# Kernel tuning notes

Hardware: AMD Instinct MI355X
Metric: run time of the kernel (lower is better)

## Reference

```python
import jax, jax.numpy as jnp
import numpy as np

N_NODES = 50000
N_EDGES = 800000
C_IN = 64
N_HEADS = 4
HEAD_DIM = 16
FC = 64


def setup_inputs() -> dict:
    key = jax.random.key(0)
    ks = jax.random.split(key, 20)
    d = {}
    d["node_input"] = jax.random.normal(ks[0], (N_NODES, C_IN), jnp.float32)
    d["node_attr"] = jnp.ones((N_NODES, 1), jnp.float32)
    d["edge_src"] = jax.random.randint(ks[1], (N_EDGES,), 0, N_NODES)
    d["edge_dst"] = jax.random.randint(ks[2], (N_EDGES,), 0, N_NODES)
    d["edge_attr"] = jax.random.normal(ks[3], (N_EDGES, 1), jnp.float32)
    d["edge_scalars"] = jax.random.normal(ks[4], (N_EDGES, FC), jnp.float32)
    d["batch"] = jnp.zeros((N_NODES,), jnp.int32)
    s = 1.0 / np.sqrt(C_IN)
    AD = N_HEADS * HEAD_DIM  # 64
    d["Wq"] = jax.random.normal(ks[5], (C_IN, AD), jnp.float32) * s
    d["bq"] = jnp.zeros((AD,), jnp.float32)
    d["W_src"] = jax.random.normal(ks[6], (C_IN, C_IN), jnp.float32) * s
    d["b_src"] = jnp.zeros((C_IN,), jnp.float32)
    d["W_dst"] = jax.random.normal(ks[7], (C_IN, C_IN), jnp.float32) * s
    d["W_fc1"] = jax.random.normal(ks[8], (FC, FC), jnp.float32) * (1.0 / np.sqrt(FC))
    d["b_fc1"] = jnp.zeros((FC,), jnp.float32)
    d["W_fc2"] = jax.random.normal(ks[9], (FC, FC), jnp.float32) * (1.0 / np.sqrt(FC))
    d["b_fc2"] = jnp.zeros((FC,), jnp.float32)
    d["W_fc3"] = jax.random.normal(ks[10], (FC, C_IN), jnp.float32) * (1.0 / np.sqrt(FC))
    d["b_fc3"] = jnp.zeros((C_IN,), jnp.float32)
    d["W_kv"] = jax.random.normal(ks[11], (C_IN, 2 * AD), jnp.float32) * s
    d["b_kv"] = jnp.zeros((2 * AD,), jnp.float32)
    d["W_proj"] = jax.random.normal(ks[12], (AD, C_IN), jnp.float32) * (1.0 / np.sqrt(AD))
    d["b_proj"] = jnp.zeros((C_IN,), jnp.float32)
    return d


def reference(node_input, node_attr, edge_src, edge_dst, edge_attr, edge_scalars, batch,
              Wq, bq, W_src, b_src, W_dst, W_fc1, b_fc1, W_fc2, b_fc2, W_fc3, b_fc3,
              W_kv, b_kv, W_proj, b_proj):
    N = node_input.shape[0]
    # query: linear -> heads -> scale (ScaleFactor for HxH 0e irreps = 1/sqrt(num_irreps))
    q = (node_input @ Wq + bq).reshape(N, N_HEADS, HEAD_DIM)
    q = q * (1.0 / jnp.sqrt(jnp.float32(HEAD_DIM)))
    # edge messages
    msg_src = node_input @ W_src + b_src
    msg_dst = node_input @ W_dst
    kv = msg_src[edge_src] + msg_dst[edge_dst]  # [E, C]
    # SeparableFCTP (scalar irreps): radial MLP -> depthwise weights, x * edge_attr, linear
    h = jax.nn.silu(edge_scalars @ W_fc1 + b_fc1)
    h = jax.nn.silu(h @ W_fc2 + b_fc2)
    w = h @ W_fc3 + b_fc3  # [E, C] depthwise TP weights
    tp = kv * edge_attr * w
    kv2 = (tp @ W_kv + b_kv).reshape(-1, 2 * N_HEADS, HEAD_DIM)
    k = kv2[:, :N_HEADS]
    v = kv2[:, N_HEADS:]
    # per-edge scores and segment softmax over incoming edges of each dst node
    alpha = jnp.einsum('ehd,ehd->eh', q[edge_dst], k)  # [E, H]
    seg_max = jax.ops.segment_max(alpha, edge_dst, num_segments=N)
    seg_max = jnp.where(jnp.isfinite(seg_max), seg_max, 0.0)
    ex = jnp.exp(alpha - seg_max[edge_dst])
    denom = jax.ops.segment_sum(ex, edge_dst, num_segments=N)
    alpha = ex / (denom[edge_dst] + 1e-16)
    # weighted scatter-sum of values
    attn = jax.ops.segment_sum(v * alpha[..., None], edge_dst, num_segments=N)
    attn = attn.reshape(N, N_HEADS * HEAD_DIM)
    return attn @ W_proj + b_proj
```

## Files before the change

### kernel.cpp

```cpp
#include <hip/hip_runtime.h>
#include <hip/hip_bf16.h>


typedef __attribute__((ext_vector_type(8))) short    bf16x8;
typedef __attribute__((ext_vector_type(4))) float    f32x4;
typedef __attribute__((ext_vector_type(4))) unsigned short ushort4v;

__device__ __forceinline__ unsigned short f2bf(float x) {
    union { float f; unsigned u; } v; v.f = x;
    unsigned r = v.u + 0x7fffu + ((v.u >> 16) & 1u);
    return (unsigned short)(r >> 16);
}

__device__ __forceinline__ int swz(int row, int k) {
    return row * 64 + (k ^ ((row & 7) << 3));
}

__device__ __forceinline__ bf16x8 ldfrag(const unsigned short* buf, int rn, int kk, int lhi) {
    return *(const bf16x8*)(buf + swz(rn, kk * 32 + lhi * 8));
}

__global__ __launch_bounds__(384)
void node_linear_kernel(const float* __restrict__ x,
                        const float* __restrict__ Wq,   const float* __restrict__ bq,
                        const float* __restrict__ Wsrc, const float* __restrict__ bsrc,
                        const float* __restrict__ Wdst,
                        float* __restrict__ qout, float* __restrict__ msout,
                        float* __restrict__ mdout, int N)
{
    __shared__ __align__(16) float sW[64 * 192];
    __shared__ float sb[192];
    __shared__ __align__(16) float xs[32][68];

    const int t = threadIdx.x;
    for (int idx4 = t; idx4 < 3072; idx4 += 384) {
        const int k  = idx4 / 48;
        const int j4 = idx4 % 48;
        const float4* src = (j4 < 16) ? (const float4*)&Wq  [k * 64 + j4 * 4]
                         : (j4 < 32) ? (const float4*)&Wsrc[k * 64 + (j4 - 16) * 4]
                                     : (const float4*)&Wdst[k * 64 + (j4 - 32) * 4];
        ((float4*)sW)[idx4] = *src;
    }
    if (t < 192) sb[t] = (t < 64) ? bq[t] : (t < 128) ? bsrc[t - 64] : 0.0f;

    const int nbase = blockIdx.x * 32;
    for (int idx = t; idx < 512; idx += 384) {
        const int n  = idx >> 4;
        const int c4 = (idx & 15) * 4;
        const int gn = nbase + n;
        float4 g = make_float4(0.f, 0.f, 0.f, 0.f);
        if (gn < N) g = *(const float4*)&x[(size_t)gn * 64 + c4];
        *(float4*)&xs[n][c4] = g;
    }
    __syncthreads();

    const int te = t / 48, tj = t % 48;
    const int j0 = tj * 4, e0 = te * 4;

    float acc[4][4];
#pragma unroll
    for (int i = 0; i < 4; ++i)
#pragma unroll
        for (int c = 0; c < 4; ++c) acc[i][c] = 0.f;

#pragma unroll 16
    for (int k = 0; k < 64; ++k) {
        const float4 wv = *(const float4*)&sW[k * 192 + j0];
        const float a0 = xs[e0 + 0][k], a1 = xs[e0 + 1][k];
        const float a2 = xs[e0 + 2][k], a3 = xs[e0 + 3][k];
        acc[0][0] += a0 * wv.x; acc[0][1] += a0 * wv.y; acc[0][2] += a0 * wv.z; acc[0][3] += a0 * wv.w;
        acc[1][0] += a1 * wv.x; acc[1][1] += a1 * wv.y; acc[1][2] += a1 * wv.z; acc[1][3] += a1 * wv.w;
        acc[2][0] += a2 * wv.x; acc[2][1] += a2 * wv.y; acc[2][2] += a2 * wv.z; acc[2][3] += a2 * wv.w;
        acc[3][0] += a3 * wv.x; acc[3][1] += a3 * wv.y; acc[3][2] += a3 * wv.z; acc[3][3] += a3 * wv.w;
    }

#pragma unroll
    for (int i = 0; i < 4; ++i) {
        const int gn = nbase + e0 + i;
        if (gn >= N) continue;
        float4 o;
        o.x = acc[i][0] + sb[j0 + 0];
        o.y = acc[i][1] + sb[j0 + 1];
        o.z = acc[i][2] + sb[j0 + 2];
        o.w = acc[i][3] + sb[j0 + 3];
        if (j0 < 64) {
            o.x *= 0.25f; o.y *= 0.25f; o.z *= 0.25f; o.w *= 0.25f;
            *(float4*)&qout[(size_t)gn * 64 + j0] = o;
        } else if (j0 < 128) {
            *(float4*)&msout[(size_t)gn * 64 + (j0 - 64)] = o;
        } else {
            *(float4*)&mdout[(size_t)gn * 64 + (j0 - 128)] = o;
        }
    }
}

__global__ __launch_bounds__(512, 4)
void edge_fused_mfma(const int* __restrict__ esrc, const int* __restrict__ edst,
                     const float* __restrict__ eattr, const float* __restrict__ escal,
                     const float* __restrict__ W1, const float* __restrict__ b1,
                     const float* __restrict__ W2, const float* __restrict__ b2,
                     const float* __restrict__ W3, const float* __restrict__ b3,
                     const float* __restrict__ Wkv, const float* __restrict__ bkv,
                     const float* __restrict__ qbuf, const float* __restrict__ msrc,
                     const float* __restrict__ mdst,
                     float* __restrict__ num, float* __restrict__ den)
{
    __shared__ __align__(16) unsigned short sh[36864];
    unsigned short* sW1t  = sh;
    unsigned short* sW2t  = sh + 4096;
    unsigned short* sW3t  = sh + 8192;
    unsigned short* sWkvt = sh + 12288;
    unsigned short* sA0   = sh + 20480;
    unsigned short* sA1   = sh + 28672;
    __shared__ float sB1[64], sB2[64], sB3[64], sBkv[128], sEa[128];
    __shared__ int   sSrc[128], sDst[128];

    const int t    = threadIdx.x;
    const int base = blockIdx.x * 128;
    const int lane = t & 63;
    const int wave = t >> 6;
    const int l15  = lane & 15;
    const int lhi  = lane >> 4;
    const int rowBase = wave * 16;

    for (int idx = t; idx < 4096; idx += 512) {
        const int k = idx >> 6, n = idx & 63;
        const int d = swz(n, k);
        sW1t[d] = f2bf(W1[idx]);
        sW2t[d] = f2bf(W2[idx]);
        sW3t[d] = f2bf(W3[idx]);
    }
    for (int idx = t; idx < 8192; idx += 512) {
        const int k = idx >> 7, n = idx & 127;
        sWkvt[swz(n, k)] = f2bf(Wkv[idx]);
    }
    for (int i4 = t; i4 < 2048; i4 += 512) {
        const int e = i4 >> 4, k4 = (i4 & 15) << 2;
        const float4 g = *(const float4*)&escal[(size_t)(base + e) * 64 + k4];
        ushort4v p = { f2bf(g.x), f2bf(g.y), f2bf(g.z), f2bf(g.w) };
        *(ushort4v*)&sA0[swz(e, k4)] = p;
    }
    if (t < 64)              { sB1[t] = b1[t]; sB2[t] = b2[t]; sB3[t] = b3[t]; }
    if (t >= 64  && t < 192) sBkv[t - 64] = bkv[t - 64];
    if (t >= 192 && t < 320) {
        const int e = t - 192;
        sSrc[e] = esrc[base + e];
        sDst[e] = edst[base + e];
        sEa[e]  = eattr[base + e];
    }
    __syncthreads();

    {
        f32x4 acc[4] = {{0,0,0,0},{0,0,0,0},{0,0,0,0},{0,0,0,0}};
#pragma unroll
        for (int kk = 0; kk < 2; ++kk) {
            const bf16x8 a = ldfrag(sA0, rowBase + l15, kk, lhi);
#pragma unroll
            for (int c = 0; c < 4; ++c) {
                const bf16x8 b = ldfrag(sW1t, c * 16 + l15, kk, lhi);
                acc[c] = __builtin_amdgcn_mfma_f32_16x16x32_bf16(a, b, acc[c], 0, 0, 0);
            }
        }
#pragma unroll
        for (int c = 0; c < 4; ++c)
#pragma unroll
            for (int r = 0; r < 4; ++r) {
                const int row = rowBase + lhi * 4 + r;
                const int col = c * 16 + l15;
                const float v = acc[c][r] + sB1[col];
                sA1[swz(row, col)] = f2bf(v / (1.f + __expf(-v)));
            }
    }
    __syncthreads();

    {
        f32x4 acc[4] = {{0,0,0,0},{0,0,0,0},{0,0,0,0},{0,0,0,0}};
#pragma unroll
        for (int kk = 0; kk < 2; ++kk) {
            const bf16x8 a = ldfrag(sA1, rowBase + l15, kk, lhi);
#pragma unroll
            for (int c = 0; c < 4; ++c) {
                const bf16x8 b = ldfrag(sW2t, c * 16 + l15, kk, lhi);
                acc[c] = __builtin_amdgcn_mfma_f32_16x16x32_bf16(a, b, acc[c], 0, 0, 0);
            }
        }
#pragma unroll
        for (int c = 0; c < 4; ++c)
#pragma unroll
            for (int r = 0; r < 4; ++r) {
                const int row = rowBase + lhi * 4 + r;
                const int col = c * 16 + l15;
                const float v = acc[c][r] + sB2[col];
                sA0[swz(row, col)] = f2bf(v / (1.f + __expf(-v)));
            }
    }
    __syncthreads();

    {
        f32x4 acc[4] = {{0,0,0,0},{0,0,0,0},{0,0,0,0},{0,0,0,0}};
#pragma unroll
        for (int kk = 0; kk < 2; ++kk) {
            const bf16x8 a = ldfrag(sA0, rowBase + l15, kk, lhi);
#pragma unroll
            for (int c = 0; c < 4; ++c) {
                const bf16x8 b = ldfrag(sW3t, c * 16 + l15, kk, lhi);
                acc[c] = __builtin_amdgcn_mfma_f32_16x16x32_bf16(a, b, acc[c], 0, 0, 0);
            }
        }
        float ms[4][4], md[4][4];
#pragma unroll
        for (int c = 0; c < 4; ++c)
#pragma unroll
            for (int r = 0; r < 4; ++r) {
                const int row = rowBase + lhi * 4 + r;
                const int col = c * 16 + l15;
                ms[c][r] = msrc[(size_t)sSrc[row] * 64 + col];
                md[c][r] = mdst[(size_t)sDst[row] * 64 + col];
            }
#pragma unroll
        for (int c = 0; c < 4; ++c)
#pragma unroll
            for (int r = 0; r < 4; ++r) {
                const int row = rowBase + lhi * 4 + r;
                const int col = c * 16 + l15;
                const float w  = acc[c][r] + sB3[col];
                const float tp = (ms[c][r] + md[c][r]) * sEa[row] * w;
                sA1[swz(row, col)] = f2bf(tp);
            }
    }
    __syncthreads();

    f32x4 acc2[8] = {{0,0,0,0},{0,0,0,0},{0,0,0,0},{0,0,0,0},
                     {0,0,0,0},{0,0,0,0},{0,0,0,0},{0,0,0,0}};
#pragma unroll
    for (int kk = 0; kk < 2; ++kk) {
        const bf16x8 a = ldfrag(sA1, rowBase + l15, kk, lhi);
#pragma unroll
        for (int c = 0; c < 8; ++c) {
            const bf16x8 b = ldfrag(sWkvt, c * 16 + l15, kk, lhi);
            acc2[c] = __builtin_amdgcn_mfma_f32_16x16x32_bf16(a, b, acc2[c], 0, 0, 0);
        }
    }

    int   gds[4];
    float qreg[4][4];
#pragma unroll
    for (int r = 0; r < 4; ++r) gds[r] = sDst[rowBase + lhi * 4 + r];
#pragma unroll
    for (int h = 0; h < 4; ++h)
#pragma unroll
        for (int r = 0; r < 4; ++r)
            qreg[h][r] = qbuf[(size_t)gds[r] * 64 + h * 16 + l15];

    float ex[4][4];
#pragma unroll
    for (int h = 0; h < 4; ++h)
#pragma unroll
        for (int r = 0; r < 4; ++r) {
            float s = (acc2[h][r] + sBkv[h * 16 + l15]) * qreg[h][r];
            s += __shfl_xor(s, 1);
            s += __shfl_xor(s, 2);
            s += __shfl_xor(s, 4);
            s += __shfl_xor(s, 8);
            const float e = __expf(s);
            ex[h][r] = e;
            if (l15 == h * 4 + r) atomicAdd(&den[(size_t)gds[r] * 4 + h], e);
        }

#pragma unroll
    for (int vt = 0; vt < 4; ++vt)
#pragma unroll
        for (int r = 0; r < 4; ++r) {
            const float vv = acc2[4 + vt][r] + sBkv[64 + vt * 16 + l15];
            atomicAdd(&num[(size_t)gds[r] * 64 + vt * 16 + l15], ex[vt][r] * vv);
        }
}

__global__ __launch_bounds__(256)
void final_proj_kernel(const float* __restrict__ num, const float* __restrict__ den,
                       const float* __restrict__ Wp, const float* __restrict__ bp,
                       float* __restrict__ out, int N)
{
    __shared__ __align__(16) float sW[64 * 64];
    __shared__ float sb[64];
    __shared__ __align__(16) float at[64][68];

    const int t = threadIdx.x;
    for (int i4 = t; i4 < 1024; i4 += 256)
        ((float4*)sW)[i4] = ((const float4*)Wp)[i4];
    if (t < 64) sb[t] = bp[t];

    const int nbase = blockIdx.x * 64;
    for (int idx = t; idx < 1024; idx += 256) {
        const int n  = idx >> 4;
        const int c4 = (idx & 15) * 4;
        const int gn = nbase + n;
        float4 g = make_float4(0.f, 0.f, 0.f, 0.f);
        if (gn < N) {
            const float4 nm = *(const float4*)&num[(size_t)gn * 64 + c4];
            const float inv = 1.0f / (den[(size_t)gn * 4 + (c4 >> 4)] + 1e-16f);
            g = make_float4(nm.x * inv, nm.y * inv, nm.z * inv, nm.w * inv);
        }
        *(float4*)&at[n][c4] = g;
    }
    __syncthreads();

    const int te = t >> 4, tj = t & 15;
    const int j0 = tj * 4, e0 = te * 4;

    float acc[4][4];
#pragma unroll
    for (int i = 0; i < 4; ++i)
#pragma unroll
        for (int c = 0; c < 4; ++c) acc[i][c] = 0.f;

#pragma unroll 16
    for (int k = 0; k < 64; ++k) {
        const float4 wv = *(const float4*)&sW[k * 64 + j0];
        const float a0 = at[e0 + 0][k], a1 = at[e0 + 1][k];
        const float a2 = at[e0 + 2][k], a3 = at[e0 + 3][k];
        acc[0][0] += a0 * wv.x; acc[0][1] += a0 * wv.y; acc[0][2] += a0 * wv.z; acc[0][3] += a0 * wv.w;
        acc[1][0] += a1 * wv.x; acc[1][1] += a1 * wv.y; acc[1][2] += a1 * wv.z; acc[1][3] += a1 * wv.w;
        acc[2][0] += a2 * wv.x; acc[2][1] += a2 * wv.y; acc[2][2] += a2 * wv.z; acc[2][3] += a2 * wv.w;
        acc[3][0] += a3 * wv.x; acc[3][1] += a3 * wv.y; acc[3][2] += a3 * wv.z; acc[3][3] += a3 * wv.w;
    }

#pragma unroll
    for (int i = 0; i < 4; ++i) {
        const int gn = nbase + e0 + i;
        if (gn >= N) continue;
        float4 o;
        o.x = acc[i][0] + sb[j0 + 0];
        o.y = acc[i][1] + sb[j0 + 1];
        o.z = acc[i][2] + sb[j0 + 2];
        o.w = acc[i][3] + sb[j0 + 3];
        *(float4*)&out[(size_t)gn * 64 + j0] = o;
    }
}

extern "C" void kernel_launch(void* const* d_in, const int* in_sizes, int n_in,
                              void* d_out, int out_size, void* d_ws, size_t ws_size,
                              hipStream_t stream)
{
    const float* node_input = (const float*)d_in[0];
    const int*   edge_src   = (const int*)  d_in[2];
    const int*   edge_dst   = (const int*)  d_in[3];
    const float* edge_attr  = (const float*)d_in[4];
    const float* edge_scal  = (const float*)d_in[5];
    const float* Wq    = (const float*)d_in[7];
    const float* bq    = (const float*)d_in[8];
    const float* W_src = (const float*)d_in[9];
    const float* b_src = (const float*)d_in[10];
    const float* W_dst = (const float*)d_in[11];
    const float* W_fc1 = (const float*)d_in[12];
    const float* b_fc1 = (const float*)d_in[13];
    const float* W_fc2 = (const float*)d_in[14];
    const float* b_fc2 = (const float*)d_in[15];
    const float* W_fc3 = (const float*)d_in[16];
    const float* b_fc3 = (const float*)d_in[17];
    const float* W_kv  = (const float*)d_in[18];
    const float* b_kv  = (const float*)d_in[19];
    const float* W_proj = (const float*)d_in[20];
    const float* b_proj = (const float*)d_in[21];

    const int N = in_sizes[0] / 64;
    const int E = in_sizes[2];

    float* ws    = (float*)d_ws;
    float* q_buf = ws;
    float* msrc  = ws + (size_t)N * 64;
    float* mdst  = ws + (size_t)N * 128;
    float* num   = ws + (size_t)N * 192;
    float* den   = ws + (size_t)N * 256;

    hipMemsetAsync(num, 0, (size_t)N * 68 * sizeof(float), stream);

    {
        dim3 grid((N + 31) / 32);
        node_linear_kernel<<<grid, 384, 0, stream>>>(node_input, Wq, bq, W_src, b_src, W_dst,
                                                     q_buf, msrc, mdst, N);
    }
    {
        dim3 grid(E / 128);
        edge_fused_mfma<<<grid, 512, 0, stream>>>(edge_src, edge_dst, edge_attr, edge_scal,
                                                  W_fc1, b_fc1, W_fc2, b_fc2, W_fc3, b_fc3,
                                                  W_kv, b_kv, q_buf, msrc, mdst, num, den);
    }
    {
        dim3 grid((N + 63) / 64);
        final_proj_kernel<<<grid, 256, 0, stream>>>(num, den, W_proj, b_proj, (float*)d_out, N);
    }
}
```

Before: 730.2 us.

## Persistent grid-stride kernels with precomputed swizzled bf16 weights

```diff
diff --git a/kernel.cpp b/kernel.cpp
--- a/kernel.cpp
+++ b/kernel.cpp
@@ -18,6 +18,27 @@
 
 __device__ __forceinline__ bf16x8 ldfrag(const unsigned short* buf, int rn, int kk, int lhi) {
     return *(const bf16x8*)(buf + swz(rn, kk * 32 + lhi * 8));
+}
+
+__global__ __launch_bounds__(256)
+void prep_weights(const float* __restrict__ W1, const float* __restrict__ W2,
+                  const float* __restrict__ W3, const float* __restrict__ Wkv,
+                  unsigned short* __restrict__ wbf)
+{
+    const int d = blockIdx.x * 256 + threadIdx.x;
+    if (d < 12288) {
+        const int w  = d >> 12;
+        const int r  = d & 4095;
+        const int n  = r >> 6, kx = r & 63;
+        const int k  = kx ^ ((n & 7) << 3);
+        const float* W = (w == 0) ? W1 : (w == 1) ? W2 : W3;
+        wbf[d] = f2bf(W[k * 64 + n]);
+    } else if (d < 20480) {
+        const int r  = d - 12288;
+        const int n  = r >> 6, kx = r & 63;
+        const int k  = kx ^ ((n & 7) << 3);
+        wbf[d] = f2bf(Wkv[k * 128 + n]);
+    }
 }
 
 __global__ __launch_bounds__(384)
@@ -26,7 +47,7 @@
                         const float* __restrict__ Wsrc, const float* __restrict__ bsrc,
                         const float* __restrict__ Wdst,
                         float* __restrict__ qout, float* __restrict__ msout,
-                        float* __restrict__ mdout, int N)
+                        float* __restrict__ mdout, int N, int ntiles)
 {
     __shared__ __align__(16) float sW[64 * 192];
     __shared__ float sb[192];
@@ -43,53 +64,56 @@
     }
     if (t < 192) sb[t] = (t < 64) ? bq[t] : (t < 128) ? bsrc[t - 64] : 0.0f;
 
-    const int nbase = blockIdx.x * 32;
-    for (int idx = t; idx < 512; idx += 384) {
-        const int n  = idx >> 4;
-        const int c4 = (idx & 15) * 4;
-        const int gn = nbase + n;
-        float4 g = make_float4(0.f, 0.f, 0.f, 0.f);
-        if (gn < N) g = *(const float4*)&x[(size_t)gn * 64 + c4];
-        *(float4*)&xs[n][c4] = g;
-    }
-    __syncthreads();
-
     const int te = t / 48, tj = t % 48;
     const int j0 = tj * 4, e0 = te * 4;
 
-    float acc[4][4];
-#pragma unroll
-    for (int i = 0; i < 4; ++i)
-#pragma unroll
-        for (int c = 0; c < 4; ++c) acc[i][c] = 0.f;
+    for (int tile = blockIdx.x; tile < ntiles; tile += gridDim.x) {
+        const int nbase = tile * 32;
+        __syncthreads();
+        for (int idx = t; idx < 512; idx += 384) {
+            const int n  = idx >> 4;
+            const int c4 = (idx & 15) * 4;
+            const int gn = nbase + n;
+            float4 g = make_float4(0.f, 0.f, 0.f, 0.f);
+            if (gn < N) g = *(const float4*)&x[(size_t)gn * 64 + c4];
+            *(float4*)&xs[n][c4] = g;
+        }
+        __syncthreads();
+
+        float acc[4][4];
+#pragma unroll
+        for (int i = 0; i < 4; ++i)
+#pragma unroll
+            for (int c = 0; c < 4; ++c) acc[i][c] = 0.f;
 
 #pragma unroll 16
-    for (int k = 0; k < 64; ++k) {
-        const float4 wv = *(const float4*)&sW[k * 192 + j0];
-        const float a0 = xs[e0 + 0][k], a1 = xs[e0 + 1][k];
-        const float a2 = xs[e0 + 2][k], a3 = xs[e0 + 3][k];
-        acc[0][0] += a0 * wv.x; acc[0][1] += a0 * wv.y; acc[0][2] += a0 * wv.z; acc[0][3] += a0 * wv.w;
-        acc[1][0] += a1 * wv.x; acc[1][1] += a1 * wv.y; acc[1][2] += a1 * wv.z; acc[1][3] += a1 * wv.w;
-        acc[2][0] += a2 * wv.x; acc[2][1] += a2 * wv.y; acc[2][2] += a2 * wv.z; acc[2][3] += a2 * wv.w;
-        acc[3][0] += a3 * wv.x; acc[3][1] += a3 * wv.y; acc[3][2] += a3 * wv.z; acc[3][3] += a3 * wv.w;
-    }
-
-#pragma unroll
-    for (int i = 0; i < 4; ++i) {
-        const int gn = nbase + e0 + i;
-        if (gn >= N) continue;
-        float4 o;
-        o.x = acc[i][0] + sb[j0 + 0];
-        o.y = acc[i][1] + sb[j0 + 1];
-        o.z = acc[i][2] + sb[j0 + 2];
-        o.w = acc[i][3] + sb[j0 + 3];
-        if (j0 < 64) {
-            o.x *= 0.25f; o.y *= 0.25f; o.z *= 0.25f; o.w *= 0.25f;
-            *(float4*)&qout[(size_t)gn * 64 + j0] = o;
-        } else if (j0 < 128) {
-            *(float4*)&msout[(size_t)gn * 64 + (j0 - 64)] = o;
-        } else {
-            *(float4*)&mdout[(size_t)gn * 64 + (j0 - 128)] = o;
+        for (int k = 0; k < 64; ++k) {
+            const float4 wv = *(const float4*)&sW[k * 192 + j0];
+            const float a0 = xs[e0 + 0][k], a1 = xs[e0 + 1][k];
+            const float a2 = xs[e0 + 2][k], a3 = xs[e0 + 3][k];
+            acc[0][0] += a0 * wv.x; acc[0][1] += a0 * wv.y; acc[0][2] += a0 * wv.z; acc[0][3] += a0 * wv.w;
+            acc[1][0] += a1 * wv.x; acc[1][1] += a1 * wv.y; acc[1][2] += a1 * wv.z; acc[1][3] += a1 * wv.w;
+            acc[2][0] += a2 * wv.x; acc[2][1] += a2 * wv.y; acc[2][2] += a2 * wv.z; acc[2][3] += a2 * wv.w;
+            acc[3][0] += a3 * wv.x; acc[3][1] += a3 * wv.y; acc[3][2] += a3 * wv.z; acc[3][3] += a3 * wv.w;
+        }
+
+#pragma unroll
+        for (int i = 0; i < 4; ++i) {
+            const int gn = nbase + e0 + i;
+            if (gn >= N) continue;
+            float4 o;
+            o.x = acc[i][0] + sb[j0 + 0];
+            o.y = acc[i][1] + sb[j0 + 1];
+            o.z = acc[i][2] + sb[j0 + 2];
+            o.w = acc[i][3] + sb[j0 + 3];
+            if (j0 < 64) {
+                o.x *= 0.25f; o.y *= 0.25f; o.z *= 0.25f; o.w *= 0.25f;
+                *(float4*)&qout[(size_t)gn * 64 + j0] = o;
+            } else if (j0 < 128) {
+                *(float4*)&msout[(size_t)gn * 64 + (j0 - 64)] = o;
+            } else {
+                *(float4*)&mdout[(size_t)gn * 64 + (j0 - 128)] = o;
+            }
         }
     }
 }
@@ -97,13 +121,12 @@
 __global__ __launch_bounds__(512, 4)
 void edge_fused_mfma(const int* __restrict__ esrc, const int* __restrict__ edst,
                      const float* __restrict__ eattr, const float* __restrict__ escal,
-                     const float* __restrict__ W1, const float* __restrict__ b1,
-                     const float* __restrict__ W2, const float* __restrict__ b2,
-                     const float* __restrict__ W3, const float* __restrict__ b3,
-                     const float* __restrict__ Wkv, const float* __restrict__ bkv,
+                     const unsigned short* __restrict__ wbf,
+                     const float* __restrict__ b1, const float* __restrict__ b2,
+                     const float* __restrict__ b3, const float* __restrict__ bkv,
                      const float* __restrict__ qbuf, const float* __restrict__ msrc,
                      const float* __restrict__ mdst,
-                     float* __restrict__ num, float* __restrict__ den)
+                     float* __restrict__ num, float* __restrict__ den, int ntiles)
 {
     __shared__ __align__(16) unsigned short sh[36864];
     unsigned short* sW1t  = sh;
@@ -116,170 +139,170 @@
     __shared__ int   sSrc[128], sDst[128];
 
     const int t    = threadIdx.x;
-    const int base = blockIdx.x * 128;
     const int lane = t & 63;
     const int wave = t >> 6;
     const int l15  = lane & 15;
     const int lhi  = lane >> 4;
     const int rowBase = wave * 16;
 
-    for (int idx = t; idx < 4096; idx += 512) {
-        const int k = idx >> 6, n = idx & 63;
-        const int d = swz(n, k);
-        sW1t[d] = f2bf(W1[idx]);
-        sW2t[d] = f2bf(W2[idx]);
-        sW3t[d] = f2bf(W3[idx]);
-    }
-    for (int idx = t; idx < 8192; idx += 512) {
-        const int k = idx >> 7, n = idx & 127;
-        sWkvt[swz(n, k)] = f2bf(Wkv[idx]);
-    }
-    for (int i4 = t; i4 < 2048; i4 += 512) {
-        const int e = i4 >> 4, k4 = (i4 & 15) << 2;
-        const float4 g = *(const float4*)&escal[(size_t)(base + e) * 64 + k4];
-        ushort4v p = { f2bf(g.x), f2bf(g.y), f2bf(g.z), f2bf(g.w) };
-        *(ushort4v*)&sA0[swz(e, k4)] = p;
-    }
+    for (int i4 = t; i4 < 2560; i4 += 512)
+        ((float4*)sh)[i4] = ((const float4*)wbf)[i4];
     if (t < 64)              { sB1[t] = b1[t]; sB2[t] = b2[t]; sB3[t] = b3[t]; }
-    if (t >= 64  && t < 192) sBkv[t - 64] = bkv[t - 64];
-    if (t >= 192 && t < 320) {
-        const int e = t - 192;
-        sSrc[e] = esrc[base + e];
-        sDst[e] = edst[base + e];
-        sEa[e]  = eattr[base + e];
-    }
-    __syncthreads();
-
-    {
-        f32x4 acc[4] = {{0,0,0,0},{0,0,0,0},{0,0,0,0},{0,0,0,0}};
-#pragma unroll
-        for (int kk = 0; kk < 2; ++kk) {
-            const bf16x8 a = ldfrag(sA0, rowBase + l15, kk, lhi);
-#pragma unroll
-            for (int c = 0; c < 4; ++c) {
-                const bf16x8 b = ldfrag(sW1t, c * 16 + l15, kk, lhi);
-                acc[c] = __builtin_amdgcn_mfma_f32_16x16x32_bf16(a, b, acc[c], 0, 0, 0);
-            }
-        }
-#pragma unroll
-        for (int c = 0; c < 4; ++c)
-#pragma unroll
-            for (int r = 0; r < 4; ++r) {
-                const int row = rowBase + lhi * 4 + r;
-                const int col = c * 16 + l15;
-                const float v = acc[c][r] + sB1[col];
-                sA1[swz(row, col)] = f2bf(v / (1.f + __expf(-v)));
-            }
-    }
-    __syncthreads();
-
-    {
-        f32x4 acc[4] = {{0,0,0,0},{0,0,0,0},{0,0,0,0},{0,0,0,0}};
+    if (t >= 64 && t < 192)  sBkv[t - 64] = bkv[t - 64];
+
+    for (int tile = blockIdx.x; tile < ntiles; tile += gridDim.x) {
+        const int base = tile * 128;
+        __syncthreads();
+
+        {
+            int e = t >> 4;
+            const int c4 = (t & 15) << 2;
+#pragma unroll
+            for (int p = 0; p < 4; ++p, e += 32) {
+                const float4 g = *(const float4*)&escal[(size_t)(base + e) * 64 + c4];
+                ushort4v pk = { f2bf(g.x), f2bf(g.y), f2bf(g.z), f2bf(g.w) };
+                *(ushort4v*)&sA0[swz(e, c4)] = pk;
+            }
+        }
+        if (t >= 192 && t < 320) {
+            const int e = t - 192;
+            sSrc[e] = esrc[base + e];
+            sDst[e] = edst[base + e];
+            sEa[e]  = eattr[base + e];
+        }
+        __syncthreads();
+
+        {
+            f32x4 acc[4] = {{0,0,0,0},{0,0,0,0},{0,0,0,0},{0,0,0,0}};
+#pragma unroll
+            for (int kk = 0; kk < 2; ++kk) {
+                const bf16x8 a = ldfrag(sA0, rowBase + l15, kk, lhi);
+#pragma unroll
+                for (int c = 0; c < 4; ++c) {
+                    const bf16x8 b = ldfrag(sW1t, c * 16 + l15, kk, lhi);
+                    acc[c] = __builtin_amdgcn_mfma_f32_16x16x32_bf16(a, b, acc[c], 0, 0, 0);
+                }
+            }
+#pragma unroll
+            for (int c = 0; c < 4; ++c)
+#pragma unroll
+                for (int r = 0; r < 4; ++r) {
+                    const int row = rowBase + lhi * 4 + r;
+                    const int col = c * 16 + l15;
+                    const float v = acc[c][r] + sB1[col];
+                    sA1[swz(row, col)] = f2bf(v / (1.f + __expf(-v)));
+                }
+        }
+        __syncthreads();
+
+        {
+            f32x4 acc[4] = {{0,0,0,0},{0,0,0,0},{0,0,0,0},{0,0,0,0}};
+#pragma unroll
+            for (int kk = 0; kk < 2; ++kk) {
+                const bf16x8 a = ldfrag(sA1, rowBase + l15, kk, lhi);
+#pragma unroll
+                for (int c = 0; c < 4; ++c) {
+                    const bf16x8 b = ldfrag(sW2t, c * 16 + l15, kk, lhi);
+                    acc[c] = __builtin_amdgcn_mfma_f32_16x16x32_bf16(a, b, acc[c], 0, 0, 0);
+                }
+            }
+#pragma unroll
+            for (int c = 0; c < 4; ++c)
+#pragma unroll
+                for (int r = 0; r < 4; ++r) {
+                    const int row = rowBase + lhi * 4 + r;
+                    const int col = c * 16 + l15;
+                    const float v = acc[c][r] + sB2[col];
+                    sA0[swz(row, col)] = f2bf(v / (1.f + __expf(-v)));
+                }
+        }
+        __syncthreads();
+
+        {
+            f32x4 acc[4] = {{0,0,0,0},{0,0,0,0},{0,0,0,0},{0,0,0,0}};
+#pragma unroll
+            for (int kk = 0; kk < 2; ++kk) {
+                const bf16x8 a = ldfrag(sA0, rowBase + l15, kk, lhi);
+#pragma unroll
+                for (int c = 0; c < 4; ++c) {
+                    const bf16x8 b = ldfrag(sW3t, c * 16 + l15, kk, lhi);
+                    acc[c] = __builtin_amdgcn_mfma_f32_16x16x32_bf16(a, b, acc[c], 0, 0, 0);
+                }
+            }
+            float ms[4][4], md[4][4];
+#pragma unroll
+            for (int c = 0; c < 4; ++c)
+#pragma unroll
+                for (int r = 0; r < 4; ++r) {
+                    const int row = rowBase + lhi * 4 + r;
+                    const int col = c * 16 + l15;
+                    ms[c][r] = msrc[(size_t)sSrc[row] * 64 + col];
+                    md[c][r] = mdst[(size_t)sDst[row] * 64 + col];
+                }
+#pragma unroll
+            for (int c = 0; c < 4; ++c)
+#pragma unroll
+                for (int r = 0; r < 4; ++r) {
+                    const int row = rowBase + lhi * 4 + r;
+                    const int col = c * 16 + l15;
+                    const float w  = acc[c][r] + sB3[col];
+                    const float tp = (ms[c][r] + md[c][r]) * sEa[row] * w;
+                    sA1[swz(row, col)] = f2bf(tp);
+                }
+        }
+        __syncthreads();
+
+        f32x4 acc2[8] = {{0,0,0,0},{0,0,0,0},{0,0,0,0},{0,0,0,0},
+                         {0,0,0,0},{0,0,0,0},{0,0,0,0},{0,0,0,0}};
 #pragma unroll
         for (int kk = 0; kk < 2; ++kk) {
             const bf16x8 a = ldfrag(sA1, rowBase + l15, kk, lhi);
 #pragma unroll
-            for (int c = 0; c < 4; ++c) {
-                const bf16x8 b = ldfrag(sW2t, c * 16 + l15, kk, lhi);
-                acc[c] = __builtin_amdgcn_mfma_f32_16x16x32_bf16(a, b, acc[c], 0, 0, 0);
-            }
-        }
-#pragma unroll
-        for (int c = 0; c < 4; ++c)
+            for (int c = 0; c < 8; ++c) {
+                const bf16x8 b = ldfrag(sWkvt, c * 16 + l15, kk, lhi);
+                acc2[c] = __builtin_amdgcn_mfma_f32_16x16x32_bf16(a, b, acc2[c], 0, 0, 0);
+            }
+        }
+
+        int   gds[4];
+        float qreg[4][4];
+#pragma unroll
+        for (int r = 0; r < 4; ++r) gds[r] = sDst[rowBase + lhi * 4 + r];
+#pragma unroll
+        for (int h = 0; h < 4; ++h)
+#pragma unroll
+            for (int r = 0; r < 4; ++r)
+                qreg[h][r] = qbuf[(size_t)gds[r] * 64 + h * 16 + l15];
+
+        float ex[4][4];
+#pragma unroll
+        for (int h = 0; h < 4; ++h)
 #pragma unroll
             for (int r = 0; r < 4; ++r) {
-                const int row = rowBase + lhi * 4 + r;
-                const int col = c * 16 + l15;
-                const float v = acc[c][r] + sB2[col];
-                sA0[swz(row, col)] = f2bf(v / (1.f + __expf(-v)));
-            }
-    }
-    __syncthreads();
-
-    {
-        f32x4 acc[4] = {{0,0,0,0},{0,0,0,0},{0,0,0,0},{0,0,0,0}};
-#pragma unroll
-        for (int kk = 0; kk < 2; ++kk) {
-            const bf16x8 a = ldfrag(sA0, rowBase + l15, kk, lhi);
-#pragma unroll
-            for (int c = 0; c < 4; ++c) {
-                const bf16x8 b = ldfrag(sW3t, c * 16 + l15, kk, lhi);
-                acc[c] = __builtin_amdgcn_mfma_f32_16x16x32_bf16(a, b, acc[c], 0, 0, 0);
-            }
-        }
-        float ms[4][4], md[4][4];
-#pragma unroll
-        for (int c = 0; c < 4; ++c)
+                float s = (acc2[h][r] + sBkv[h * 16 + l15]) * qreg[h][r];
+                s += __shfl_xor(s, 1);
+                s += __shfl_xor(s, 2);
+                s += __shfl_xor(s, 4);
+                s += __shfl_xor(s, 8);
+                const float e = __expf(s);
+                ex[h][r] = e;
+                if (l15 == h * 4 + r) atomicAdd(&den[(size_t)gds[r] * 4 + h], e);
+            }
+
+#pragma unroll
+        for (int vt = 0; vt < 4; ++vt)
 #pragma unroll
             for (int r = 0; r < 4; ++r) {
-                const int row = rowBase + lhi * 4 + r;
-                const int col = c * 16 + l15;
-                ms[c][r] = msrc[(size_t)sSrc[row] * 64 + col];
-                md[c][r] = mdst[(size_t)sDst[row] * 64 + col];
-            }
-#pragma unroll
-        for (int c = 0; c < 4; ++c)
-#pragma unroll
-            for (int r = 0; r < 4; ++r) {
-                const int row = rowBase + lhi * 4 + r;
-                const int col = c * 16 + l15;
-                const float w  = acc[c][r] + sB3[col];
-                const float tp = (ms[c][r] + md[c][r]) * sEa[row] * w;
-                sA1[swz(row, col)] = f2bf(tp);
-            }
-    }
-    __syncthreads();
-
-    f32x4 acc2[8] = {{0,0,0,0},{0,0,0,0},{0,0,0,0},{0,0,0,0},
-                     {0,0,0,0},{0,0,0,0},{0,0,0,0},{0,0,0,0}};
-#pragma unroll
-    for (int kk = 0; kk < 2; ++kk) {
-        const bf16x8 a = ldfrag(sA1, rowBase + l15, kk, lhi);
-#pragma unroll
-        for (int c = 0; c < 8; ++c) {
-            const bf16x8 b = ldfrag(sWkvt, c * 16 + l15, kk, lhi);
-            acc2[c] = __builtin_amdgcn_mfma_f32_16x16x32_bf16(a, b, acc2[c], 0, 0, 0);
-        }
-    }
-
-    int   gds[4];
-    float qreg[4][4];
-#pragma unroll
-    for (int r = 0; r < 4; ++r) gds[r] = sDst[rowBase + lhi * 4 + r];
-#pragma unroll
-    for (int h = 0; h < 4; ++h)
-#pragma unroll
-        for (int r = 0; r < 4; ++r)
-            qreg[h][r] = qbuf[(size_t)gds[r] * 64 + h * 16 + l15];
-
-    float ex[4][4];
-#pragma unroll
-    for (int h = 0; h < 4; ++h)
-#pragma unroll
-        for (int r = 0; r < 4; ++r) {
-            float s = (acc2[h][r] + sBkv[h * 16 + l15]) * qreg[h][r];
-            s += __shfl_xor(s, 1);
-            s += __shfl_xor(s, 2);
-            s += __shfl_xor(s, 4);
-            s += __shfl_xor(s, 8);
-            const float e = __expf(s);
-            ex[h][r] = e;
-            if (l15 == h * 4 + r) atomicAdd(&den[(size_t)gds[r] * 4 + h], e);
-        }
-
-#pragma unroll
-    for (int vt = 0; vt < 4; ++vt)
-#pragma unroll
-        for (int r = 0; r < 4; ++r) {
-            const float vv = acc2[4 + vt][r] + sBkv[64 + vt * 16 + l15];
-            atomicAdd(&num[(size_t)gds[r] * 64 + vt * 16 + l15], ex[vt][r] * vv);
-        }
+                const float vv = acc2[4 + vt][r] + sBkv[64 + vt * 16 + l15];
+                atomicAdd(&num[(size_t)gds[r] * 64 + vt * 16 + l15], ex[vt][r] * vv);
+            }
+    }
 }
 
 __global__ __launch_bounds__(256)
 void final_proj_kernel(const float* __restrict__ num, const float* __restrict__ den,
                        const float* __restrict__ Wp, const float* __restrict__ bp,
-                       float* __restrict__ out, int N)
+                       float* __restrict__ out, int N, int ntiles)
 {
     __shared__ __align__(16) float sW[64 * 64];
     __shared__ float sb[64];
@@ -290,51 +313,54 @@
         ((float4*)sW)[i4] = ((const float4*)Wp)[i4];
     if (t < 64) sb[t] = bp[t];
 
-    const int nbase = blockIdx.x * 64;
-    for (int idx = t; idx < 1024; idx += 256) {
-        const int n  = idx >> 4;
-        const int c4 = (idx & 15) * 4;
-        const int gn = nbase + n;
-        float4 g = make_float4(0.f, 0.f, 0.f, 0.f);
-        if (gn < N) {
-            const float4 nm = *(const float4*)&num[(size_t)gn * 64 + c4];
-            const float inv = 1.0f / (den[(size_t)gn * 4 + (c4 >> 4)] + 1e-16f);
-            g = make_float4(nm.x * inv, nm.y * inv, nm.z * inv, nm.w * inv);
-        }
-        *(float4*)&at[n][c4] = g;
-    }
-    __syncthreads();
-
     const int te = t >> 4, tj = t & 15;
     const int j0 = tj * 4, e0 = te * 4;
 
-    float acc[4][4];
-#pragma unroll
-    for (int i = 0; i < 4; ++i)
-#pragma unroll
-        for (int c = 0; c < 4; ++c) acc[i][c] = 0.f;
+    for (int tile = blockIdx.x; tile < ntiles; tile += gridDim.x) {
+        const int nbase = tile * 64;
+        __syncthreads();
+        for (int idx = t; idx < 1024; idx += 256) {
+            const int n  = idx >> 4;
+            const int c4 = (idx & 15) * 4;
+            const int gn = nbase + n;
+            float4 g = make_float4(0.f, 0.f, 0.f, 0.f);
+            if (gn < N) {
+                const float4 nm = *(const float4*)&num[(size_t)gn * 64 + c4];
+                const float inv = 1.0f / (den[(size_t)gn * 4 + (c4 >> 4)] + 1e-16f);
+                g = make_float4(nm.x * inv, nm.y * inv, nm.z * inv, nm.w * inv);
+            }
+            *(float4*)&at[n][c4] = g;
+        }
+        __syncthreads();
+
+        float acc[4][4];
+#pragma unroll
+        for (int i = 0; i < 4; ++i)
+#pragma unroll
+            for (int c = 0; c < 4; ++c) acc[i][c] = 0.f;
 
 #pragma unroll 16
-    for (int k = 0; k < 64; ++k) {
-        const float4 wv = *(const float4*)&sW[k * 64 + j0];
-        const float a0 = at[e0 + 0][k], a1 = at[e0 + 1][k];
-        const float a2 = at[e0 + 2][k], a3 = at[e0 + 3][k];
-        acc[0][0] += a0 * wv.x; acc[0][1] += a0 * wv.y; acc[0][2] += a0 * wv.z; acc[0][3] += a0 * wv.w;
-        acc[1][0] += a1 * wv.x; acc[1][1] += a1 * wv.y; acc[1][2] += a1 * wv.z; acc[1][3] += a1 * wv.w;
-        acc[2][0] += a2 * wv.x; acc[2][1] += a2 * wv.y; acc[2][2] += a2 * wv.z; acc[2][3] += a2 * wv.w;
-        acc[3][0] += a3 * wv.x; acc[3][1] += a3 * wv.y; acc[3][2] += a3 * wv.z; acc[3][3] += a3 * wv.w;
-    }
-
-#pragma unroll
-    for (int i = 0; i < 4; ++i) {
-        const int gn = nbase + e0 + i;
-        if (gn >= N) continue;
-        float4 o;
-        o.x = acc[i][0] + sb[j0 + 0];
-        o.y = acc[i][1] + sb[j0 + 1];
-        o.z = acc[i][2] + sb[j0 + 2];
-        o.w = acc[i][3] + sb[j0 + 3];
-        *(float4*)&out[(size_t)gn * 64 + j0] = o;
+        for (int k = 0; k < 64; ++k) {
+            const float4 wv = *(const float4*)&sW[k * 64 + j0];
+            const float a0 = at[e0 + 0][k], a1 = at[e0 + 1][k];
+            const float a2 = at[e0 + 2][k], a3 = at[e0 + 3][k];
+            acc[0][0] += a0 * wv.x; acc[0][1] += a0 * wv.y; acc[0][2] += a0 * wv.z; acc[0][3] += a0 * wv.w;
+            acc[1][0] += a1 * wv.x; acc[1][1] += a1 * wv.y; acc[1][2] += a1 * wv.z; acc[1][3] += a1 * wv.w;
+            acc[2][0] += a2 * wv.x; acc[2][1] += a2 * wv.y; acc[2][2] += a2 * wv.z; acc[2][3] += a2 * wv.w;
+            acc[3][0] += a3 * wv.x; acc[3][1] += a3 * wv.y; acc[3][2] += a3 * wv.z; acc[3][3] += a3 * wv.w;
+        }
+
+#pragma unroll
+        for (int i = 0; i < 4; ++i) {
+            const int gn = nbase + e0 + i;
+            if (gn >= N) continue;
+            float4 o;
+            o.x = acc[i][0] + sb[j0 + 0];
+            o.y = acc[i][1] + sb[j0 + 1];
+            o.z = acc[i][2] + sb[j0 + 2];
+            o.w = acc[i][3] + sb[j0 + 3];
+            *(float4*)&out[(size_t)gn * 64 + j0] = o;
+        }
     }
 }
 
@@ -372,22 +398,26 @@
     float* mdst  = ws + (size_t)N * 128;
     float* num   = ws + (size_t)N * 192;
     float* den   = ws + (size_t)N * 256;
+    unsigned short* wbf = (unsigned short*)(ws + (size_t)N * 260);
 
     hipMemsetAsync(num, 0, (size_t)N * 68 * sizeof(float), stream);
 
+    prep_weights<<<80, 256, 0, stream>>>(W_fc1, W_fc2, W_fc3, W_kv, wbf);
+
     {
-        dim3 grid((N + 31) / 32);
-        node_linear_kernel<<<grid, 384, 0, stream>>>(node_input, Wq, bq, W_src, b_src, W_dst,
-                                                     q_buf, msrc, mdst, N);
+        const int ntiles = (N + 31) / 32;
+        node_linear_kernel<<<512, 384, 0, stream>>>(node_input, Wq, bq, W_src, b_src, W_dst,
+                                                    q_buf, msrc, mdst, N, ntiles);
     }
     {
-        dim3 grid(E / 128);
-        edge_fused_mfma<<<grid, 512, 0, stream>>>(edge_src, edge_dst, edge_attr, edge_scal,
-                                                  W_fc1, b_fc1, W_fc2, b_fc2, W_fc3, b_fc3,
-                                                  W_kv, b_kv, q_buf, msrc, mdst, num, den);
+        const int ntiles = E / 128;
+        edge_fused_mfma<<<512, 512, 0, stream>>>(edge_src, edge_dst, edge_attr, edge_scal,
+                                                 wbf, b_fc1, b_fc2, b_fc3, b_kv,
+                                                 q_buf, msrc, mdst, num, den, ntiles);
     }
     {
-        dim3 grid((N + 63) / 64);
-        final_proj_kernel<<<grid, 256, 0, stream>>>(num, den, W_proj, b_proj, (float*)d_out, N);
-    }
-}
+        const int ntiles = (N + 63) / 64;
+        final_proj_kernel<<<512, 256, 0, stream>>>(num, den, W_proj, b_proj,
+                                                   (float*)d_out, N, ntiles);
+    }
+}
```

After: 672.2 us. 1.09x faster.
